# Kernel optimization log

Hardware: AMD Instinct MI355X
Metric: run time of the kernel (lower is better)

Reference implementation:

```python
import jax, jax.numpy as jnp
import numpy as np

N, D = 8192, 256
L = 4            # num residual quantizer levels
K = 1024         # codes per codebook
E = 8            # num experts
BETA = 1.0

sg = jax.lax.stop_gradient


def setup_inputs() -> dict:
    key = jax.random.key(0)
    k1, k2, k3, k4, k5 = jax.random.split(key, 5)
    x = jax.random.normal(k1, (N, D), dtype=jnp.float32)
    labels = jax.random.randint(k2, (L, N), 0, 100)
    # learned params
    codebooks = jax.random.normal(k3, (L, E, K, D), dtype=jnp.float32) * 0.02
    gate_W = jax.random.normal(k4, (D, E), dtype=jnp.float32) * (1.0 / np.sqrt(D))
    gate_b = jnp.zeros((E,), dtype=jnp.float32)
    return {"x": x, "labels": labels, "codebooks": codebooks,
            "gate_W": gate_W, "gate_b": gate_b}


def reference(x, labels, codebooks, gate_W, gate_b):
    # MoE gate computed once on the initial residual (= x), as in the source
    gate_probs = jax.nn.softmax(x @ gate_W + gate_b, axis=-1)      # [N, E]
    expert_id = jnp.argmax(gate_probs, axis=-1)                     # [N]

    residual = x
    x_q = jnp.zeros_like(x)
    all_losses = []
    all_indices = []
    for l in range(L):
        cb = codebooks[l]                                           # [E, K, D]
        # squared-distance argmin: ||c||^2 - 2 r.c (||r||^2 constant per row)
        dots = jnp.einsum('nd,ekd->enk', residual, cb)              # [E, N, K]
        c2 = jnp.sum(cb * cb, axis=-1)                              # [E, K]
        dist = c2[:, None, :] - 2.0 * dots                          # [E, N, K]
        idx_all = jnp.argmin(dist, axis=-1)                         # [E, N]
        idx = jnp.take_along_axis(idx_all, expert_id[None, :], axis=0)[0]  # [N]
        quant = cb[expert_id, idx]                                  # [N, D]
        # codebook + commitment loss
        loss = jnp.mean((sg(quant) - residual) ** 2) \
             + BETA * jnp.mean((quant - sg(residual)) ** 2)
        # straight-through estimator
        q_st = residual + sg(quant - residual)
        residual = residual - q_st
        x_q = x_q + q_st
        all_losses.append(loss)
        all_indices.append(idx)

    all_indices.append(expert_id)
    mean_losses = jnp.mean(jnp.stack(all_losses))
    indices = jnp.stack(all_indices, axis=-1)                       # [N, L+1]
    return (x_q, mean_losses, indices)
```

## Files before the change

kernel.cpp:

```cpp
#include <hip/hip_runtime.h>
#include <stdint.h>

#define N 8192
#define D 256
#define L 4
#define K 1024
#define E 8

#define TM 128
#define TN 128
#define BK 32
#define KSPLIT (K / TN)
#define MAXTILES (N / TM + E)
#define TH 4e-4f
#define MAXC 96

typedef unsigned long long u64;
typedef __attribute__((ext_vector_type(8))) short bf16x8;
typedef __attribute__((ext_vector_type(4))) float f32x4;

__device__ __forceinline__ unsigned f2sort(float f) {
    unsigned u = __float_as_uint(f);
    return (u & 0x80000000u) ? ~u : (u | 0x80000000u);
}
__device__ __forceinline__ float sort2f(unsigned s) {
    unsigned u = (s & 0x80000000u) ? (s & 0x7fffffffu) : ~s;
    return __uint_as_float(u);
}
__device__ __forceinline__ u64 umin64(u64 a, u64 b) { return a < b ? a : b; }
__device__ __forceinline__ u64 umax64(u64 a, u64 b) { return a > b ? a : b; }

__device__ __forceinline__ unsigned short f2bf(float f) {
    unsigned u = __float_as_uint(f);
    unsigned r = (u + 0x7fffu + ((u >> 16) & 1u)) >> 16;
    return (unsigned short)r;
}
__device__ __forceinline__ float bf2f(unsigned short h) {
    return __uint_as_float(((unsigned)h) << 16);
}

__device__ __forceinline__ void gload_lds16(const void* g, void* l) {
    __builtin_amdgcn_global_load_lds(
        (const __attribute__((address_space(1))) unsigned int*)(g),
        (__attribute__((address_space(3))) unsigned int*)(l), 16, 0, 0);
}

__device__ __forceinline__ float exact_dist(const float* __restrict__ crow,
                                            const float* __restrict__ rrow,
                                            float c2v) {
    float dot = 0.f;
    for (int d0 = 0; d0 < D; d0 += 4) {
        float4 c4 = *reinterpret_cast<const float4*>(crow + d0);
        float4 s4 = *reinterpret_cast<const float4*>(rrow + d0);
        dot = fmaf(s4.x, c4.x, dot);
        dot = fmaf(s4.y, c4.y, dot);
        dot = fmaf(s4.z, c4.z, dot);
        dot = fmaf(s4.w, c4.w, dot);
    }
    return c2v - 2.0f * dot;
}

__global__ void gate_kernel(const float* __restrict__ x,
                            const float* __restrict__ gW,
                            const float* __restrict__ gb,
                            int* __restrict__ eid,
                            float* __restrict__ out_idx,
                            unsigned short* __restrict__ rhi,
                            unsigned short* __restrict__ rlo) {
    int wid = threadIdx.x >> 6, lane = threadIdx.x & 63;
    int n = blockIdx.x * 4 + wid;
    float4 xv = *reinterpret_cast<const float4*>(x + (size_t)n * D + lane * 4);

    ushort4 h4, l4;
    h4.x = f2bf(xv.x); l4.x = f2bf(xv.x - bf2f(h4.x));
    h4.y = f2bf(xv.y); l4.y = f2bf(xv.y - bf2f(h4.y));
    h4.z = f2bf(xv.z); l4.z = f2bf(xv.z - bf2f(h4.z));
    h4.w = f2bf(xv.w); l4.w = f2bf(xv.w - bf2f(h4.w));
    *reinterpret_cast<ushort4*>(rhi + (size_t)n * D + lane * 4) = h4;
    *reinterpret_cast<ushort4*>(rlo + (size_t)n * D + lane * 4) = l4;

    float xa[4] = {xv.x, xv.y, xv.z, xv.w};
    float a[8];
#pragma unroll
    for (int e = 0; e < 8; e++) a[e] = 0.f;
    const float* wr = gW + (size_t)(lane * 4) * E;
#pragma unroll
    for (int i = 0; i < 4; i++) {
        float xs = xa[i];
        float4 w0 = *reinterpret_cast<const float4*>(wr + i * E);
        float4 w1 = *reinterpret_cast<const float4*>(wr + i * E + 4);
        a[0] = fmaf(xs, w0.x, a[0]); a[1] = fmaf(xs, w0.y, a[1]);
        a[2] = fmaf(xs, w0.z, a[2]); a[3] = fmaf(xs, w0.w, a[3]);
        a[4] = fmaf(xs, w1.x, a[4]); a[5] = fmaf(xs, w1.y, a[5]);
        a[6] = fmaf(xs, w1.z, a[6]); a[7] = fmaf(xs, w1.w, a[7]);
    }
#pragma unroll
    for (int off = 32; off > 0; off >>= 1) {
#pragma unroll
        for (int e = 0; e < 8; e++) a[e] += __shfl_xor(a[e], off);
    }
    if (lane == 0) {
        int be = 0;
        float bv = a[0] + gb[0];
        for (int e = 1; e < 8; e++) {
            float v = a[e] + gb[e];
            if (v > bv) { bv = v; be = e; }
        }
        eid[n] = be;
        out_idx[(size_t)n * (L + 1) + L] = (float)be;
    }
}

__global__ __launch_bounds__(256)
void bucket_kernel(const int* __restrict__ eid, int* __restrict__ counts,
                   int* __restrict__ order) {
    __shared__ u64 wtot_lo[4], wtot_hi[4];
    __shared__ int base[E];
    int tid = threadIdx.x, lane = tid & 63, wv = tid >> 6;
    int n0 = tid * 32;
    int eids[32];
    u64 lo = 0, hi = 0;
#pragma unroll
    for (int j = 0; j < 32; j++) {
        int e = eid[n0 + j];
        eids[j] = e;
        if (e < 4) lo += 1ull << (e * 16);
        else       hi += 1ull << ((e - 4) * 16);
    }
    u64 slo = lo, shi = hi;
#pragma unroll
    for (int d = 1; d < 64; d <<= 1) {
        u64 t1 = __shfl_up(slo, d);
        u64 t2 = __shfl_up(shi, d);
        if (lane >= d) { slo += t1; shi += t2; }
    }
    if (lane == 63) { wtot_lo[wv] = slo; wtot_hi[wv] = shi; }
    __syncthreads();
    u64 wofflo = 0, woffhi = 0;
    for (int w = 0; w < wv; w++) { wofflo += wtot_lo[w]; woffhi += wtot_hi[w]; }
    u64 exlo = wofflo + slo - lo;
    u64 exhi = woffhi + shi - hi;
    if (tid == 0) {
        u64 tlo = wtot_lo[0] + wtot_lo[1] + wtot_lo[2] + wtot_lo[3];
        u64 thi = wtot_hi[0] + wtot_hi[1] + wtot_hi[2] + wtot_hi[3];
        int a = 0;
#pragma unroll
        for (int e = 0; e < 4; e++) {
            int c = (int)((tlo >> (e * 16)) & 0xffff);
            counts[e] = c; base[e] = a; a += c;
        }
#pragma unroll
        for (int e = 0; e < 4; e++) {
            int c = (int)((thi >> (e * 16)) & 0xffff);
            counts[4 + e] = c; base[4 + e] = a; a += c;
        }
    }
    __syncthreads();
#pragma unroll
    for (int j = 0; j < 32; j++) {
        int e = eids[j];
        int p;
        if (e < 4) { p = (int)((exlo >> (e * 16)) & 0xffff); exlo += 1ull << (e * 16); }
        else       { p = (int)((exhi >> ((e - 4) * 16)) & 0xffff); exhi += 1ull << ((e - 4) * 16); }
        order[base[e] + p] = n0 + j;
    }
}

__global__ void cb_prep(const float* __restrict__ cbs, float* __restrict__ c2,
                        unsigned short* __restrict__ cbhi,
                        unsigned short* __restrict__ cblo) {
    int wid = threadIdx.x >> 6, lane = threadIdx.x & 63;
    size_t row = (size_t)blockIdx.x * 4 + wid;
    float4 v = *reinterpret_cast<const float4*>(cbs + row * D + lane * 4);
    ushort4 h4, l4;
    h4.x = f2bf(v.x); l4.x = f2bf(v.x - bf2f(h4.x));
    h4.y = f2bf(v.y); l4.y = f2bf(v.y - bf2f(h4.y));
    h4.z = f2bf(v.z); l4.z = f2bf(v.z - bf2f(h4.z));
    h4.w = f2bf(v.w); l4.w = f2bf(v.w - bf2f(h4.w));
    *reinterpret_cast<ushort4*>(cbhi + row * D + lane * 4) = h4;
    *reinterpret_cast<ushort4*>(cblo + row * D + lane * 4) = l4;
    float s = v.x * v.x + v.y * v.y + v.z * v.z + v.w * v.w;
#pragma unroll
    for (int off = 32; off > 0; off >>= 1) s += __shfl_xor(s, off);
    if (lane == 0) c2[row] = s;
}

__global__ __launch_bounds__(256, 2)
void dist_kernel(const unsigned short* __restrict__ rhi,
                 const unsigned short* __restrict__ rlo,
                 const unsigned short* __restrict__ cbhi,
                 const unsigned short* __restrict__ cblo,
                 const float* __restrict__ c2l,
                 const int* __restrict__ order, const int* __restrict__ counts,
                 uint4* __restrict__ ws2) {
    __shared__ short lA[2][TM * 64];
    __shared__ short lB[2][TN * 64];

    int bx = blockIdx.x;
    int tile = bx >> 3, kc = bx & 7;

    int eoffL[E + 1]; int a = 0;
#pragma unroll
    for (int i = 0; i < E; i++) { eoffL[i] = a; a += counts[i]; }
    eoffL[E] = a;

    int e = -1, lt = 0, cnt = 0, cum = 0;
    for (int i = 0; i < E; i++) {
        int c = counts[i];
        int t = (c + TM - 1) / TM;
        if (tile < cum + t) { e = i; lt = tile - cum; cnt = c; break; }
        cum += t;
    }
    if (e < 0) return;
    int base = eoffL[e] + lt * TM;
    int mcnt = min(TM, cnt - lt * TM);
    int k0 = kc * TN;

    int tid = threadIdx.x;
    int lane = tid & 63, wv = tid >> 6;
    int wr = wv >> 1, wc = wv & 1;

    int srow[4], scol[4], nid[4];
#pragma unroll
    for (int i = 0; i < 4; i++) {
        int s = i * 256 + tid;
        srow[i] = s >> 3;
        scol[i] = (s & 7) ^ (srow[i] & 7);
        nid[i] = 0;
    }
#pragma unroll
    for (int i = 0; i < 4; i++) nid[i] = order[min(base + srow[i], N - 1)];

    const size_t cbbase = ((size_t)e * K + k0) * D;

    f32x4 acc[4][4];
#pragma unroll
    for (int fr = 0; fr < 4; fr++)
#pragma unroll
        for (int fc = 0; fc < 4; fc++)
            acc[fr][fc] = (f32x4){0.f, 0.f, 0.f, 0.f};

    auto STAGE = [&](int buf, int ck) {
        int dc = ck * BK;
#pragma unroll
        for (int i = 0; i < 4; i++) {
            int s = i * 256 + tid, c = scol[i];
            const unsigned short* src = (c < 4)
                ? (rhi + (size_t)nid[i] * D + dc + c * 8)
                : (rlo + (size_t)nid[i] * D + dc + (c - 4) * 8);
            gload_lds16(src, &lA[buf][s * 8]);
        }
#pragma unroll
        for (int i = 0; i < 4; i++) {
            int s = i * 256 + tid, c = scol[i];
            const unsigned short* src = (c < 4)
                ? (cbhi + cbbase + (size_t)srow[i] * D + dc + c * 8)
                : (cblo + cbbase + (size_t)srow[i] * D + dc + (c - 4) * 8);
            gload_lds16(src, &lB[buf][s * 8]);
        }
    };

    int q = lane >> 4, rL = lane & 15;
    STAGE(0, 0);
    for (int ck = 0; ck < D / BK; ck++) {
        __syncthreads();
        if (ck < D / BK - 1) STAGE((ck + 1) & 1, ck + 1);
        int buf = ck & 1;
        bf16x8 ah[4], al[4];
#pragma unroll
        for (int fr = 0; fr < 4; fr++) {
            int row = wr * 64 + fr * 16 + rL;
            ah[fr] = *reinterpret_cast<const bf16x8*>(&lA[buf][row * 64 + ((q) ^ (row & 7)) * 8]);
            al[fr] = *reinterpret_cast<const bf16x8*>(&lA[buf][row * 64 + ((4 + q) ^ (row & 7)) * 8]);
        }
#pragma unroll
        for (int fc = 0; fc < 4; fc++) {
            int row = wc * 64 + fc * 16 + rL;
            bf16x8 bh = *reinterpret_cast<const bf16x8*>(&lB[buf][row * 64 + ((q) ^ (row & 7)) * 8]);
            bf16x8 bl = *reinterpret_cast<const bf16x8*>(&lB[buf][row * 64 + ((4 + q) ^ (row & 7)) * 8]);
#pragma unroll
            for (int fr = 0; fr < 4; fr++) {
                acc[fr][fc] = __builtin_amdgcn_mfma_f32_16x16x32_bf16(ah[fr], bh, acc[fr][fc], 0, 0, 0);
                acc[fr][fc] = __builtin_amdgcn_mfma_f32_16x16x32_bf16(ah[fr], bl, acc[fr][fc], 0, 0, 0);
                acc[fr][fc] = __builtin_amdgcn_mfma_f32_16x16x32_bf16(al[fr], bh, acc[fr][fc], 0, 0, 0);
            }
        }
    }

    int cL = lane & 15;
#pragma unroll
    for (int fr = 0; fr < 4; fr++) {
#pragma unroll
        for (int j = 0; j < 4; j++) {
            int row_local = wr * 64 + fr * 16 + q * 4 + j;
            u64 best = ~0ull; unsigned sec = 0xFFFFFFFFu;
#pragma unroll
            for (int fc = 0; fc < 4; fc++) {
                int col = k0 + wc * 64 + fc * 16 + cL;
                float dist = c2l[e * K + col] - 2.0f * acc[fr][fc][j];
                u64 kk = ((u64)f2sort(dist) << 32) | (unsigned)col;
                u64 mx = umax64(best, kk);
                best = umin64(best, kk);
                sec = min(sec, (unsigned)(mx >> 32));
            }
#pragma unroll
            for (int m = 1; m < 16; m <<= 1) {
                u64 ob = __shfl_xor(best, m, 16);
                unsigned os = __shfl_xor(sec, m, 16);
                u64 mx = umax64(best, ob);
                best = umin64(best, ob);
                sec = min(min(sec, os), (unsigned)(mx >> 32));
            }
            if (cL == 0 && row_local < mcnt) {
                int n = order[base + row_local];
                uint4 v;
                v.x = (unsigned)(best & 0xffffffffu);
                v.y = (unsigned)(best >> 32);
                v.z = sec; v.w = 0;
                ws2[(size_t)n * 16 + kc * 2 + wc] = v;
            }
        }
    }
}

__global__ __launch_bounds__(256)
void finalize_kernel(const float* __restrict__ rin, float* __restrict__ resid,
                     const float* __restrict__ cbl, const uint4* __restrict__ ws2,
                     const int* __restrict__ eid, const float* __restrict__ x,
                     float* __restrict__ out, float* __restrict__ lossb,
                     const float* __restrict__ c2l,
                     unsigned short* __restrict__ rhi,
                     unsigned short* __restrict__ rlo, int l) {
    __shared__ int s_idx[4];
    __shared__ int s_eid[4];
    __shared__ float s_bd[4];
    __shared__ int s_flag[4];
    __shared__ int s_fcount;
    __shared__ int s_cand[MAXC];
    __shared__ u64 s_res[MAXC];
    __shared__ int s_nc;
    __shared__ unsigned s_scanmask;
    __shared__ int s_base;
    __shared__ u64 s_rb[4];
    __shared__ float s_ls[4];

    int tid = threadIdx.x, lane = tid & 63, wv = tid >> 6;
    int n0 = blockIdx.x * 4;
    if (tid == 0) s_fcount = 0;
    __syncthreads();

    if (wv == 0) {
        int sloc = lane >> 4;
        int n = n0 + sloc;
        int l16 = lane & 15;
        uint4 ev = ws2[(size_t)n * 16 + l16];
        u64 best = ((u64)ev.y << 32) | ev.x;
        float mybest = sort2f(ev.y);
        float mysec = sort2f(ev.z);
#pragma unroll
        for (int m = 1; m < 16; m <<= 1)
            best = umin64(best, __shfl_xor(best, m, 16));
        float bd = sort2f((unsigned)(best >> 32));
        u64 b1 = __ballot(mybest <= bd + TH);
        u64 b2 = __ballot(mysec <= bd + TH);
        if (l16 == 0) {
            s_idx[sloc] = (int)(best & 0xffffffffu);
            s_eid[sloc] = eid[n];
            s_bd[sloc] = bd;
            unsigned m1 = (unsigned)(b1 >> (sloc * 16)) & 0xFFFFu;
            unsigned m2 = (unsigned)(b2 >> (sloc * 16)) & 0xFFFFu;
            if (__popc(m1) > 1 || m2 != 0) {
                int p = atomicAdd(&s_fcount, 1);
                s_flag[p] = sloc;
            }
        }
    }
    __syncthreads();
    int fc = s_fcount;

    for (int f = 0; f < fc; f++) {
        int sloc = s_flag[f];
        int n = n0 + sloc, e = s_eid[sloc];
        float bd = s_bd[sloc];
        const float* rrow = rin + (size_t)n * D;
        if (tid == 0) { s_nc = 0; s_scanmask = 0; }
        __syncthreads();
        if (tid < 16) {
            uint4 ev = ws2[(size_t)n * 16 + tid];
            if (sort2f(ev.y) <= bd + TH) {
                int p = atomicAdd(&s_nc, 1);
                if (p < MAXC) s_cand[p] = (int)ev.x;
            }
            if (sort2f(ev.z) <= bd + TH)
                atomicOr(&s_scanmask, 1u << tid);
        }
        __syncthreads();
        unsigned sm = s_scanmask;
        while (sm) {
            int c = __ffs(sm) - 1; sm &= sm - 1;
            if (tid == 0) s_base = atomicAdd(&s_nc, 64);
            __syncthreads();
            if (tid < 64 && s_base + tid < MAXC) {
                int half = tid >> 5;
                s_cand[s_base + tid] = (c >> 1) * TN + (c & 1) * 64 + (half * 32) + (tid & 31);
            }
            __syncthreads();
        }
        __syncthreads();
        int nc = s_nc;
        if (nc > MAXC) {
            u64 rb = ~0ull;
            for (int c = 0; c < 4; c++) {
                int k = c * 256 + tid;
                float dist = exact_dist(cbl + ((size_t)e * K + k) * D, rrow,
                                        c2l[e * K + k]);
                rb = umin64(rb, ((u64)f2sort(dist) << 32) | (unsigned)k);
            }
#pragma unroll
            for (int m = 1; m < 64; m <<= 1) rb = umin64(rb, __shfl_xor(rb, m));
            if (lane == 0) s_rb[wv] = rb;
            __syncthreads();
            if (tid == 0) {
                rb = umin64(umin64(s_rb[0], s_rb[1]), umin64(s_rb[2], s_rb[3]));
                s_idx[sloc] = (int)(rb & 0xffffffffu);
            }
            __syncthreads();
        } else {
            if (tid < nc) {
                int k = s_cand[tid];
                float dist = exact_dist(cbl + ((size_t)e * K + k) * D, rrow,
                                        c2l[e * K + k]);
                s_res[tid] = ((u64)f2sort(dist) << 32) | (unsigned)k;
            }
            __syncthreads();
            if (tid == 0) {
                u64 rb = ~0ull;
                for (int i = 0; i < nc; i++) rb = umin64(rb, s_res[i]);
                s_idx[sloc] = (int)(rb & 0xffffffffu);
            }
            __syncthreads();
        }
    }

    int sloc = wv, f4p = lane;
    int n = n0 + sloc;
    int e = s_eid[sloc], idx = s_idx[sloc];
    const float* qrow = cbl + ((size_t)e * K + idx) * D;
    float4 q4 = *reinterpret_cast<const float4*>(qrow + f4p * 4);
    float4 r4 = *reinterpret_cast<const float4*>(rin + (size_t)n * D + f4p * 4);
    float dx = q4.x - r4.x, dy = q4.y - r4.y, dz = q4.z - r4.z, dw = q4.w - r4.w;
    float lsum = dx * dx + dy * dy + dz * dz + dw * dw;
    float4 nr = make_float4(r4.x - q4.x, r4.y - q4.y, r4.z - q4.z, r4.w - q4.w);
    if (l < L - 1) {
        *reinterpret_cast<float4*>(resid + (size_t)n * D + f4p * 4) = nr;
        ushort4 h4, l4w;
        h4.x = f2bf(nr.x); l4w.x = f2bf(nr.x - bf2f(h4.x));
        h4.y = f2bf(nr.y); l4w.y = f2bf(nr.y - bf2f(h4.y));
        h4.z = f2bf(nr.z); l4w.z = f2bf(nr.z - bf2f(h4.z));
        h4.w = f2bf(nr.w); l4w.w = f2bf(nr.w - bf2f(h4.w));
        *reinterpret_cast<ushort4*>(rhi + (size_t)n * D + f4p * 4) = h4;
        *reinterpret_cast<ushort4*>(rlo + (size_t)n * D + f4p * 4) = l4w;
    } else {
        float4 x4 = *reinterpret_cast<const float4*>(x + (size_t)n * D + f4p * 4);
        float4 xq = make_float4(x4.x - nr.x, x4.y - nr.y, x4.z - nr.z, x4.w - nr.w);
        *reinterpret_cast<float4*>(out + (size_t)n * D + f4p * 4) = xq;
    }
    if (f4p == 0)
        out[(size_t)N * D + 1 + (size_t)n * (L + 1) + l] = (float)idx;
#pragma unroll
    for (int m = 1; m < 64; m <<= 1) lsum += __shfl_xor(lsum, m);
    if (lane == 0) s_ls[wv] = lsum;
    __syncthreads();
    if (tid == 0)
        atomicAdd(&lossb[(blockIdx.x & 31) * 32], s_ls[0] + s_ls[1] + s_ls[2] + s_ls[3]);
}

__global__ void loss_fin_kernel(const float* __restrict__ lossb, float* __restrict__ out) {
    float s = 0.f;
    for (int i = 0; i < 32; i++) s += lossb[i * 32];
    out[(size_t)N * D] = 2.0f * s / ((float)N * (float)D * (float)L);
}

extern "C" void kernel_launch(void* const* d_in, const int* in_sizes, int n_in,
                              void* d_out, int out_size, void* d_ws, size_t ws_size,
                              hipStream_t stream) {
    const float* x   = (const float*)d_in[0];
    const float* cbs = (const float*)d_in[2];
    const float* gW  = (const float*)d_in[3];
    const float* gb  = (const float*)d_in[4];
    float* out = (float*)d_out;

    char* ws = (char*)d_ws;
    float*          resid = (float*)(ws);
    unsigned short* rhi   = (unsigned short*)(ws + 8388608);
    unsigned short* rlo   = (unsigned short*)(ws + 12582912);
    unsigned short* cbhi  = (unsigned short*)(ws + 16777216);
    unsigned short* cblo  = (unsigned short*)(ws + 33554432);
    float*          c2    = (float*)(ws + 50331648);
    int*            eid   = (int*)(ws + 50462720);
    int*            order = (int*)(ws + 50495488);
    uint4*          ws2   = (uint4*)(ws + 50528768);
    char*           smallp = ws + 52625920;
    int*   counts  = (int*)(smallp);
    float* lossb   = (float*)(smallp + 128);

    hipMemsetAsync(smallp, 0, 4352, stream);

    gate_kernel<<<N / 4, 256, 0, stream>>>(x, gW, gb, eid,
                                           out + (size_t)N * D + 1, rhi, rlo);
    bucket_kernel<<<1, 256, 0, stream>>>(eid, counts, order);
    cb_prep<<<(L * E * K) / 4, 256, 0, stream>>>(cbs, c2, cbhi, cblo);

    for (int l = 0; l < L; l++) {
        const float* rin = (l == 0) ? x : resid;
        size_t cboff = (size_t)l * E * K * D;
        const float* c2l = c2 + (size_t)l * E * K;
        dist_kernel<<<MAXTILES * KSPLIT, 256, 0, stream>>>(
            rhi, rlo, cbhi + cboff, cblo + cboff, c2l, order, counts, ws2);
        finalize_kernel<<<N / 4, 256, 0, stream>>>(
            rin, resid, cbs + cboff, ws2, eid, x, out, lossb, c2l, rhi, rlo, l);
    }
    loss_fin_kernel<<<1, 1, 0, stream>>>(lossb, out);
}
```

Before: 320.7 us.

## Drop bf16 hi/lo split for single-bf16 distance GEMM with wider exact rescore

Replaces the three-MFMA split-bf16 (hi*hi + hi*lo + lo*hi) distance computation with a single bf16 MFMA per tile. It removes the lo buffers for residuals and codebooks and halves the LDS tiles, which allows more blocks per CU. To keep argmin exact despite the coarser distances, the candidate threshold and the max candidate count for fp32 rescoring are widened. The change cuts GEMM compute and memory traffic roughly threefold, at the cost of more exact-distance rescoring in finalize and a risk of overflowing the candidate buffer.

```diff
diff --git a/kernel.cpp b/kernel.cpp
--- a/kernel.cpp
+++ b/kernel.cpp
@@ -12,8 +12,8 @@
 #define BK 32
 #define KSPLIT (K / TN)
 #define MAXTILES (N / TM + E)
-#define TH 4e-4f
-#define MAXC 96
+#define TH 0.06f
+#define MAXC 224
 
 typedef unsigned long long u64;
 typedef __attribute__((ext_vector_type(8))) short bf16x8;
@@ -34,9 +34,6 @@
     unsigned u = __float_as_uint(f);
     unsigned r = (u + 0x7fffu + ((u >> 16) & 1u)) >> 16;
     return (unsigned short)r;
-}
-__device__ __forceinline__ float bf2f(unsigned short h) {
-    return __uint_as_float(((unsigned)h) << 16);
 }
 
 __device__ __forceinline__ void gload_lds16(const void* g, void* l) {
@@ -65,19 +62,14 @@
                             const float* __restrict__ gb,
                             int* __restrict__ eid,
                             float* __restrict__ out_idx,
-                            unsigned short* __restrict__ rhi,
-                            unsigned short* __restrict__ rlo) {
+                            unsigned short* __restrict__ rhi) {
     int wid = threadIdx.x >> 6, lane = threadIdx.x & 63;
     int n = blockIdx.x * 4 + wid;
     float4 xv = *reinterpret_cast<const float4*>(x + (size_t)n * D + lane * 4);
 
-    ushort4 h4, l4;
-    h4.x = f2bf(xv.x); l4.x = f2bf(xv.x - bf2f(h4.x));
-    h4.y = f2bf(xv.y); l4.y = f2bf(xv.y - bf2f(h4.y));
-    h4.z = f2bf(xv.z); l4.z = f2bf(xv.z - bf2f(h4.z));
-    h4.w = f2bf(xv.w); l4.w = f2bf(xv.w - bf2f(h4.w));
+    ushort4 h4;
+    h4.x = f2bf(xv.x); h4.y = f2bf(xv.y); h4.z = f2bf(xv.z); h4.w = f2bf(xv.w);
     *reinterpret_cast<ushort4*>(rhi + (size_t)n * D + lane * 4) = h4;
-    *reinterpret_cast<ushort4*>(rlo + (size_t)n * D + lane * 4) = l4;
 
     float xa[4] = {xv.x, xv.y, xv.z, xv.w};
     float a[8];
@@ -167,34 +159,27 @@
 }
 
 __global__ void cb_prep(const float* __restrict__ cbs, float* __restrict__ c2,
-                        unsigned short* __restrict__ cbhi,
-                        unsigned short* __restrict__ cblo) {
+                        unsigned short* __restrict__ cbhi) {
     int wid = threadIdx.x >> 6, lane = threadIdx.x & 63;
     size_t row = (size_t)blockIdx.x * 4 + wid;
     float4 v = *reinterpret_cast<const float4*>(cbs + row * D + lane * 4);
-    ushort4 h4, l4;
-    h4.x = f2bf(v.x); l4.x = f2bf(v.x - bf2f(h4.x));
-    h4.y = f2bf(v.y); l4.y = f2bf(v.y - bf2f(h4.y));
-    h4.z = f2bf(v.z); l4.z = f2bf(v.z - bf2f(h4.z));
-    h4.w = f2bf(v.w); l4.w = f2bf(v.w - bf2f(h4.w));
+    ushort4 h4;
+    h4.x = f2bf(v.x); h4.y = f2bf(v.y); h4.z = f2bf(v.z); h4.w = f2bf(v.w);
     *reinterpret_cast<ushort4*>(cbhi + row * D + lane * 4) = h4;
-    *reinterpret_cast<ushort4*>(cblo + row * D + lane * 4) = l4;
     float s = v.x * v.x + v.y * v.y + v.z * v.z + v.w * v.w;
 #pragma unroll
     for (int off = 32; off > 0; off >>= 1) s += __shfl_xor(s, off);
     if (lane == 0) c2[row] = s;
 }
 
-__global__ __launch_bounds__(256, 2)
+__global__ __launch_bounds__(256, 4)
 void dist_kernel(const unsigned short* __restrict__ rhi,
-                 const unsigned short* __restrict__ rlo,
                  const unsigned short* __restrict__ cbhi,
-                 const unsigned short* __restrict__ cblo,
                  const float* __restrict__ c2l,
                  const int* __restrict__ order, const int* __restrict__ counts,
                  uint4* __restrict__ ws2) {
-    __shared__ short lA[2][TM * 64];
-    __shared__ short lB[2][TN * 64];
+    __shared__ short lA[2][TM * 32];
+    __shared__ short lB[2][TN * 32];
 
     int bx = blockIdx.x;
     int tile = bx >> 3, kc = bx & 7;
@@ -220,16 +205,15 @@
     int lane = tid & 63, wv = tid >> 6;
     int wr = wv >> 1, wc = wv & 1;
 
-    int srow[4], scol[4], nid[4];
-#pragma unroll
-    for (int i = 0; i < 4; i++) {
+    int srow[2], scol[2], nid[2];
+#pragma unroll
+    for (int i = 0; i < 2; i++) {
         int s = i * 256 + tid;
-        srow[i] = s >> 3;
-        scol[i] = (s & 7) ^ (srow[i] & 7);
-        nid[i] = 0;
-    }
-#pragma unroll
-    for (int i = 0; i < 4; i++) nid[i] = order[min(base + srow[i], N - 1)];
+        srow[i] = s >> 2;
+        scol[i] = (s & 3) ^ ((srow[i] >> 1) & 3);
+    }
+#pragma unroll
+    for (int i = 0; i < 2; i++) nid[i] = order[min(base + srow[i], N - 1)];
 
     const size_t cbbase = ((size_t)e * K + k0) * D;
 
@@ -243,20 +227,16 @@
     auto STAGE = [&](int buf, int ck) {
         int dc = ck * BK;
 #pragma unroll
-        for (int i = 0; i < 4; i++) {
-            int s = i * 256 + tid, c = scol[i];
-            const unsigned short* src = (c < 4)
-                ? (rhi + (size_t)nid[i] * D + dc + c * 8)
-                : (rlo + (size_t)nid[i] * D + dc + (c - 4) * 8);
-            gload_lds16(src, &lA[buf][s * 8]);
-        }
-#pragma unroll
-        for (int i = 0; i < 4; i++) {
-            int s = i * 256 + tid, c = scol[i];
-            const unsigned short* src = (c < 4)
-                ? (cbhi + cbbase + (size_t)srow[i] * D + dc + c * 8)
-                : (cblo + cbbase + (size_t)srow[i] * D + dc + (c - 4) * 8);
-            gload_lds16(src, &lB[buf][s * 8]);
+        for (int i = 0; i < 2; i++) {
+            int s = i * 256 + tid;
+            gload_lds16(rhi + (size_t)nid[i] * D + dc + scol[i] * 8,
+                        &lA[buf][s * 8]);
+        }
+#pragma unroll
+        for (int i = 0; i < 2; i++) {
+            int s = i * 256 + tid;
+            gload_lds16(cbhi + cbbase + (size_t)srow[i] * D + dc + scol[i] * 8,
+                        &lB[buf][s * 8]);
         }
     };
 
@@ -266,24 +246,22 @@
         __syncthreads();
         if (ck < D / BK - 1) STAGE((ck + 1) & 1, ck + 1);
         int buf = ck & 1;
-        bf16x8 ah[4], al[4];
+        bf16x8 ah[4];
 #pragma unroll
         for (int fr = 0; fr < 4; fr++) {
             int row = wr * 64 + fr * 16 + rL;
-            ah[fr] = *reinterpret_cast<const bf16x8*>(&lA[buf][row * 64 + ((q) ^ (row & 7)) * 8]);
-            al[fr] = *reinterpret_cast<const bf16x8*>(&lA[buf][row * 64 + ((4 + q) ^ (row & 7)) * 8]);
+            ah[fr] = *reinterpret_cast<const bf16x8*>(
+                &lA[buf][row * 32 + ((q ^ ((row >> 1) & 3))) * 8]);
         }
 #pragma unroll
         for (int fc = 0; fc < 4; fc++) {
             int row = wc * 64 + fc * 16 + rL;
-            bf16x8 bh = *reinterpret_cast<const bf16x8*>(&lB[buf][row * 64 + ((q) ^ (row & 7)) * 8]);
-            bf16x8 bl = *reinterpret_cast<const bf16x8*>(&lB[buf][row * 64 + ((4 + q) ^ (row & 7)) * 8]);
-#pragma unroll
-            for (int fr = 0; fr < 4; fr++) {
-                acc[fr][fc] = __builtin_amdgcn_mfma_f32_16x16x32_bf16(ah[fr], bh, acc[fr][fc], 0, 0, 0);
-                acc[fr][fc] = __builtin_amdgcn_mfma_f32_16x16x32_bf16(ah[fr], bl, acc[fr][fc], 0, 0, 0);
-                acc[fr][fc] = __builtin_amdgcn_mfma_f32_16x16x32_bf16(al[fr], bh, acc[fr][fc], 0, 0, 0);
-            }
+            bf16x8 bh = *reinterpret_cast<const bf16x8*>(
+                &lB[buf][row * 32 + ((q ^ ((row >> 1) & 3))) * 8]);
+#pragma unroll
+            for (int fr = 0; fr < 4; fr++)
+                acc[fr][fc] = __builtin_amdgcn_mfma_f32_16x16x32_bf16(
+                    ah[fr], bh, acc[fr][fc], 0, 0, 0);
         }
     }
 
@@ -329,8 +307,7 @@
                      const int* __restrict__ eid, const float* __restrict__ x,
                      float* __restrict__ out, float* __restrict__ lossb,
                      const float* __restrict__ c2l,
-                     unsigned short* __restrict__ rhi,
-                     unsigned short* __restrict__ rlo, int l) {
+                     unsigned short* __restrict__ rhi, int l) {
     __shared__ int s_idx[4];
     __shared__ int s_eid[4];
     __shared__ float s_bd[4];
@@ -400,10 +377,8 @@
             int c = __ffs(sm) - 1; sm &= sm - 1;
             if (tid == 0) s_base = atomicAdd(&s_nc, 64);
             __syncthreads();
-            if (tid < 64 && s_base + tid < MAXC) {
-                int half = tid >> 5;
-                s_cand[s_base + tid] = (c >> 1) * TN + (c & 1) * 64 + (half * 32) + (tid & 31);
-            }
+            if (tid < 64 && s_base + tid < MAXC)
+                s_cand[s_base + tid] = c * 64 + tid;
             __syncthreads();
         }
         __syncthreads();
@@ -453,13 +428,9 @@
     float4 nr = make_float4(r4.x - q4.x, r4.y - q4.y, r4.z - q4.z, r4.w - q4.w);
     if (l < L - 1) {
         *reinterpret_cast<float4*>(resid + (size_t)n * D + f4p * 4) = nr;
-        ushort4 h4, l4w;
-        h4.x = f2bf(nr.x); l4w.x = f2bf(nr.x - bf2f(h4.x));
-        h4.y = f2bf(nr.y); l4w.y = f2bf(nr.y - bf2f(h4.y));
-        h4.z = f2bf(nr.z); l4w.z = f2bf(nr.z - bf2f(h4.z));
-        h4.w = f2bf(nr.w); l4w.w = f2bf(nr.w - bf2f(h4.w));
+        ushort4 h4;
+        h4.x = f2bf(nr.x); h4.y = f2bf(nr.y); h4.z = f2bf(nr.z); h4.w = f2bf(nr.w);
         *reinterpret_cast<ushort4*>(rhi + (size_t)n * D + f4p * 4) = h4;
-        *reinterpret_cast<ushort4*>(rlo + (size_t)n * D + f4p * 4) = l4w;
     } else {
         float4 x4 = *reinterpret_cast<const float4*>(x + (size_t)n * D + f4p * 4);
         float4 xq = make_float4(x4.x - nr.x, x4.y - nr.y, x4.z - nr.z, x4.w - nr.w);
@@ -493,32 +464,30 @@
     char* ws = (char*)d_ws;
     float*          resid = (float*)(ws);
     unsigned short* rhi   = (unsigned short*)(ws + 8388608);
-    unsigned short* rlo   = (unsigned short*)(ws + 12582912);
-    unsigned short* cbhi  = (unsigned short*)(ws + 16777216);
-    unsigned short* cblo  = (unsigned short*)(ws + 33554432);
-    float*          c2    = (float*)(ws + 50331648);
-    int*            eid   = (int*)(ws + 50462720);
-    int*            order = (int*)(ws + 50495488);
-    uint4*          ws2   = (uint4*)(ws + 50528768);
-    char*           smallp = ws + 52625920;
+    unsigned short* cbhi  = (unsigned short*)(ws + 12582912);
+    float*          c2    = (float*)(ws + 29360128);
+    int*            eid   = (int*)(ws + 29491200);
+    int*            order = (int*)(ws + 29523968);
+    uint4*          ws2   = (uint4*)(ws + 29557248);
+    char*           smallp = ws + 31654400;
     int*   counts  = (int*)(smallp);
     float* lossb   = (float*)(smallp + 128);
 
     hipMemsetAsync(smallp, 0, 4352, stream);
 
     gate_kernel<<<N / 4, 256, 0, stream>>>(x, gW, gb, eid,
-                                           out + (size_t)N * D + 1, rhi, rlo);
+                                           out + (size_t)N * D + 1, rhi);
     bucket_kernel<<<1, 256, 0, stream>>>(eid, counts, order);
-    cb_prep<<<(L * E * K) / 4, 256, 0, stream>>>(cbs, c2, cbhi, cblo);
+    cb_prep<<<(L * E * K) / 4, 256, 0, stream>>>(cbs, c2, cbhi);
 
     for (int l = 0; l < L; l++) {
         const float* rin = (l == 0) ? x : resid;
         size_t cboff = (size_t)l * E * K * D;
         const float* c2l = c2 + (size_t)l * E * K;
         dist_kernel<<<MAXTILES * KSPLIT, 256, 0, stream>>>(
-            rhi, rlo, cbhi + cboff, cblo + cboff, c2l, order, counts, ws2);
+            rhi, cbhi + cboff, c2l, order, counts, ws2);
         finalize_kernel<<<N / 4, 256, 0, stream>>>(
-            rin, resid, cbs + cboff, ws2, eid, x, out, lossb, c2l, rhi, rlo, l);
+            rin, resid, cbs + cboff, ws2, eid, x, out, lossb, c2l, rhi, l);
     }
     loss_fin_kernel<<<1, 1, 0, stream>>>(lossb, out);
 }
```

New measurement: 323.0 us. No clear change (+0.7%).
